# Performance work log

Measured on AMD Instinct MI355X. Metric: run time of the kernel, lower is better.

The kernel has to match this reference:

```python
import jax, jax.numpy as jnp
import numpy as np

D_MODEL = 128
D_STATE = 64
L = 1024
BATCH = 32
DT_MIN, DT_MAX = 1e-3, 1e-1

# poly6 Chebyshev coeffs for GELU on domain [-5, 15]
POLY6_GELU = [6.04831644882, 8.094460228971, 1.371512430522, -0.740775295685,
              0.134773988002, 0.126019270103, -0.239569101196]
GELU_LO, GELU_HI = -5.0, 15.0


def cheb_eval(x, coeffs, lo, hi):
    t = (2.0 * x - (hi + lo)) / (hi - lo)
    t0 = jnp.ones_like(t)
    res = coeffs[0] * t0
    t1 = t
    res = res + coeffs[1] * t1
    for i in range(2, len(coeffs)):
        ti = 2.0 * t * t1 - t0
        res = res + coeffs[i] * ti
        t0, t1 = t1, ti
    return res


def setup_inputs() -> dict:
    key = jax.random.key(0)
    ks = jax.random.split(key, 8)
    u = jax.random.normal(ks[0], (BATCH, D_MODEL, L), dtype=jnp.float32)
    # S4DKernel params
    log_dt = jax.random.uniform(ks[1], (D_MODEL,), dtype=jnp.float32) * (np.log(DT_MAX) - np.log(DT_MIN)) + np.log(DT_MIN)
    log_A_real = jnp.log(0.5 * jnp.ones((D_MODEL, D_STATE), dtype=jnp.float32))
    A_imag = jnp.pi * jnp.tile(jnp.arange(D_STATE, dtype=jnp.float32), (D_MODEL, 1))
    B_re = jnp.ones((D_MODEL, D_STATE), dtype=jnp.float32)
    B_im = jnp.zeros((D_MODEL, D_STATE), dtype=jnp.float32)
    C_re = jax.random.normal(ks[2], (D_MODEL, D_STATE), dtype=jnp.float32)
    C_im = jax.random.normal(ks[3], (D_MODEL, D_STATE), dtype=jnp.float32)
    # block params
    D = jax.random.normal(ks[4], (D_MODEL,), dtype=jnp.float32)
    W1 = jax.random.normal(ks[5], (2 * D_MODEL, D_MODEL), dtype=jnp.float32) * (1.0 / np.sqrt(D_MODEL))
    b1 = jnp.zeros((2 * D_MODEL,), dtype=jnp.float32)
    Wdec = jax.random.normal(ks[6], (1, D_MODEL), dtype=jnp.float32) * (1.0 / np.sqrt(D_MODEL))
    bdec = jnp.zeros((1,), dtype=jnp.float32)
    return {"u": u, "log_dt": log_dt, "log_A_real": log_A_real, "A_imag": A_imag,
            "B_re": B_re, "B_im": B_im, "C_re": C_re, "C_im": C_im,
            "D": D, "W1": W1, "b1": b1, "Wdec": Wdec, "bdec": bdec}


def s4d_kernel(log_dt, log_A_real, A_imag, B_re, B_im, C_re, C_im, length):
    dt = jnp.exp(log_dt)                                  # (d,)
    A = -jnp.exp(log_A_real) + 1j * A_imag                # (d, n) complex
    A_bar = jnp.exp(A * dt[:, None])                      # (d, n)
    Bc = B_re + 1j * B_im
    Cc = C_re + 1j * C_im
    B_bar = (A_bar - 1.0) / A * Bc                        # (d, n)
    t = jnp.arange(length, dtype=jnp.float32)
    # A_bar ** t for integer t == exp(A * dt * t)  (branch cut cancels at integers)
    A_bar_pow = jnp.exp((A * dt[:, None])[:, :, None] * t)  # (d, n, L)
    K = jnp.sum(Cc[:, :, None] * A_bar_pow * B_bar[:, :, None], axis=1)  # (d, L)
    return jnp.real(K).astype(jnp.float32)


def reference(u, log_dt, log_A_real, A_imag, B_re, B_im, C_re, C_im, D, W1, b1, Wdec, bdec):
    d_model = u.shape[1]
    length = u.shape[2]
    K = s4d_kernel(log_dt, log_A_real, A_imag, B_re, B_im, C_re, C_im, length)  # (d, L)
    # torch F.conv1d(padding=L-1, groups=d)[..., :L] == left-padded depthwise cross-correlation
    conv = jax.lax.conv_general_dilated(
        u, K[:, None, :], window_strides=(1,), padding=[(length - 1, 0)],
        dimension_numbers=("NCH", "OIH", "NCH"), feature_group_count=d_model)  # (B, d, L)
    skip = conv + u * D[:, None]
    post_gelu = cheb_eval(skip, POLY6_GELU, GELU_LO, GELU_HI)
    # 1x1 conv to 2*d channels
    pre_gate = jnp.einsum("od,bdl->bol", W1, post_gelu) + b1[None, :, None]  # (B, 2d, L)
    a, b = jnp.split(pre_gate, 2, axis=1)
    gate = jnp.clip(0.25 * b + 0.5, 0.0, 1.0)  # linear_gate GLU
    gated = a * gate                            # (B, d, L)
    pooled = gated.mean(axis=-1)                # (B, d)
    return pooled @ Wdec.T + bdec               # (B, 1)
```

## Files before the change

### kernel.cpp

```cpp
#include <hip/hip_runtime.h>
#include <hip/hip_bf16.h>
#include <math.h>

#define D_MODEL 128
#define D_STATE 64
#define LEN 1024
#define BATCH 32
#define KC_STRIDE 1056

typedef short short8 __attribute__((ext_vector_type(8)));
typedef short short4v __attribute__((ext_vector_type(4)));
typedef float f32x4 __attribute__((ext_vector_type(4)));

__device__ __forceinline__ float gelu_cheb(float x) {
    float t = (2.0f * x - 10.0f) * 0.05f;
    float r = 6.04831644882f + 8.094460228971f * t;
    float tm1 = 1.0f, tc = t;
    float t2 = 2.0f * t * tc - tm1; r += 1.371512430522f  * t2;
    float t3 = 2.0f * t * t2 - tc;  r += -0.740775295685f * t3;
    float t4 = 2.0f * t * t3 - t2;  r += 0.134773988002f  * t4;
    float t5 = 2.0f * t * t4 - t3;  r += 0.126019270103f  * t5;
    float t6 = 2.0f * t * t5 - t4;  r += -0.239569101196f * t6;
    return r;
}

__device__ __forceinline__ unsigned f2bf(float f) {
    unsigned u = __float_as_uint(f);
    return (u + 0x7FFFu + ((u >> 16) & 1u)) >> 16;
}

__device__ __forceinline__ float bf2f(short s) {
    return __uint_as_float(((unsigned)(unsigned short)s) << 16);
}

__global__ __launch_bounds__(256) void k_genK3(const float* __restrict__ log_dt,
                                               const float* __restrict__ log_A_real,
                                               const float* __restrict__ A_imag,
                                               const float* __restrict__ B_re,
                                               const float* __restrict__ B_im,
                                               const float* __restrict__ C_re,
                                               const float* __restrict__ C_im,
                                               const float* __restrict__ W1,
                                               const float* __restrict__ u,
                                               short* __restrict__ w1bf,
                                               short* __restrict__ u_bf,
                                               float* __restrict__ K) {
    __shared__ float Ls[128][68];
    int bid = blockIdx.x;
    int d = bid >> 3, oct = bid & 7;
    int t = threadIdx.x;

    if (t < 32) { int i = bid * 32 + t; w1bf[i] = (short)f2bf(W1[i]); }

    {
        size_t tid = (size_t)bid * 256 + t;
        const float4* src = (const float4*)(u + tid * 16);
        float4 a = src[0], b4 = src[1], c4 = src[2], d4 = src[3];
        uint4 o0, o1;
        o0.x = f2bf(a.x)  | (f2bf(a.y)  << 16);
        o0.y = f2bf(a.z)  | (f2bf(a.w)  << 16);
        o0.z = f2bf(b4.x) | (f2bf(b4.y) << 16);
        o0.w = f2bf(b4.z) | (f2bf(b4.w) << 16);
        o1.x = f2bf(c4.x) | (f2bf(c4.y) << 16);
        o1.y = f2bf(c4.z) | (f2bf(c4.w) << 16);
        o1.z = f2bf(d4.x) | (f2bf(d4.y) << 16);
        o1.w = f2bf(d4.z) | (f2bf(d4.w) << 16);
        uint4* dst = (uint4*)u_bf + tid * 2;
        dst[0] = o0; dst[1] = o1;
    }

    int w = t >> 6, lane = t & 63;
    int idx = d * D_STATE + lane;
    float dt  = expf(log_dt[d]);
    float Are = -expf(log_A_real[idx]);
    float Aim = A_imag[idx];
    float dre = Are * dt, dim = Aim * dt;
    float e = expf(dre);
    float sn, cs; sincosf(dim, &sn, &cs);
    float zre = e * cs, zim = e * sn;
    float numr = zre - 1.0f, numi = zim;
    float inv = 1.0f / (Are * Are + Aim * Aim);
    float qr = (numr * Are + numi * Aim) * inv;
    float qi = (numi * Are - numr * Aim) * inv;
    float Br = B_re[idx], Bi = B_im[idx];
    float Bbr = qr * Br - qi * Bi;
    float Bbi = qr * Bi + qi * Br;
    float Cr = C_re[idx], Ci = C_im[idx];
    float ar = Cr * Bbr - Ci * Bbi;
    float ai = Cr * Bbi + Ci * Bbr;

    int L0 = oct * 128 + w * 32;
    float fl0 = (float)L0;
    float pre = 0.f, pim = 0.f;
    if (dre * fl0 > -30.f) {
        float e0 = expf(dre * fl0);
        float s0, c0; sincosf(dim * fl0, &s0, &c0);
        pre = e0 * (ar * c0 - ai * s0);
        pim = e0 * (ar * s0 + ai * c0);
    }

    int row0 = w * 32;
#pragma unroll
    for (int r = 0; r < 32; ++r) {
        Ls[row0 + r][lane] = pre;
        float nre = pre * zre - pim * zim;
        pim = pre * zim + pim * zre;
        pre = nre;
    }
    __syncthreads();

    if (t < 128) {
        f32x4 s4 = (f32x4){0.f, 0.f, 0.f, 0.f};
#pragma unroll
        for (int c = 0; c < 16; ++c) s4 += *(const f32x4*)&Ls[t][4 * c];
        K[(size_t)d * LEN + oct * 128 + t] = s4.x + s4.y + s4.z + s4.w;
    }
}

__global__ __launch_bounds__(256) void k_conv3(const float* __restrict__ K,
                                               const short* __restrict__ u_bf,
                                               const float* __restrict__ Dp,
                                               short* __restrict__ pgT) {
    __shared__ __align__(16) short Kc[8 * KC_STRIDE];
    int bid = blockIdx.x;
    int d  = bid >> 3;
    int nh = (bid >> 2) & 1;
    int sq = bid & 3;
    int t = threadIdx.x;

    if (t < 160) {
        int c = t / 20, y = t - c * 20;
        ((unsigned*)&Kc[c * KC_STRIDE + 1016])[y] = 0u;
    }
    {
        const float* kp = K + (size_t)d * LEN;
        float4 kv = ((const float4*)kp)[t];
        float vals[4] = {kv.x, kv.y, kv.z, kv.w};
#pragma unroll
        for (int mm = 0; mm < 4; ++mm) {
            int ei = 4 * t + mm;
            short bv = (short)f2bf(vals[mm]);
#pragma unroll
            for (int c = 0; c < 8; ++c) {
                int x = ei - c;
                if (x >= 0) Kc[c * KC_STRIDE + x] = bv;
            }
        }
    }
    __syncthreads();

    int wvu = __builtin_amdgcn_readfirstlane(t >> 6);
    int lane = t & 63;
    int m16 = lane & 15, q = lane >> 4;
    int cc = (7 - m16) & 7;
    const short* Krow = Kc + cc * KC_STRIDE;
    const short* ub = u_bf + (((size_t)(nh * 16 + m16) * D_MODEL + d) << 10);

    int x0[4];
    f32x4 accv[4];
#pragma unroll
    for (int j = 0; j < 4; ++j) {
        int I = sq + 4 * (wvu + 4 * j);
        x0[j] = 1023 + 8 * q - 16 * I - m16 - cc;
        accv[j] = (f32x4){0.f, 0.f, 0.f, 0.f};
    }

    int ks_end = (sq + 4 * wvu + 48) / 2 + 1;
    if (ks_end > 32) ks_end = 32;
    for (int ks = 0; ks < ks_end; ++ks) {
        short8 bfrag = *(const short8*)&ub[32 * ks + 8 * q];
#pragma unroll
        for (int j = 0; j < 4; ++j) {
            int I = sq + 4 * (wvu + 4 * j);
            if (2 * ks <= I) {
                short8 afrag = *(const short8*)&Krow[x0[j] + 32 * ks];
                accv[j] = __builtin_amdgcn_mfma_f32_16x16x32_bf16(afrag, bfrag, accv[j], 0, 0, 0);
            }
        }
    }

    float Dd = Dp[d];
    int b = nh * 16 + m16;
#pragma unroll
    for (int j = 0; j < 4; ++j) {
        int I = sq + 4 * (wvu + 4 * j);
        int l0 = 16 * I + 4 * q;
        short4v us = *(const short4v*)&ub[l0];
        float v0 = gelu_cheb(accv[j][0] + bf2f(us[0]) * Dd);
        float v1 = gelu_cheb(accv[j][1] + bf2f(us[1]) * Dd);
        float v2 = gelu_cheb(accv[j][2] + bf2f(us[2]) * Dd);
        float v3 = gelu_cheb(accv[j][3] + bf2f(us[3]) * Dd);
        size_t basep = ((size_t)b * LEN + l0) * D_MODEL + d;
        pgT[basep + 0 * D_MODEL] = (short)f2bf(v0);
        pgT[basep + 1 * D_MODEL] = (short)f2bf(v1);
        pgT[basep + 2 * D_MODEL] = (short)f2bf(v2);
        pgT[basep + 3 * D_MODEL] = (short)f2bf(v3);
    }
}

__global__ __launch_bounds__(256) void k_glu_mfma(const short* __restrict__ pgT,
                                                  const short* __restrict__ w1bf,
                                                  const float* __restrict__ b1,
                                                  const float* __restrict__ Wdec,
                                                  float* __restrict__ acc2) {
    __shared__ float red[4];
    int b = blockIdx.y;
    int lc = blockIdx.x;
    int l0 = lc * 64;
    int t = threadIdx.x;
    int wv = t >> 6, lane = t & 63;
    int m = lane & 15, q = lane >> 4;

    const short* wA0 = w1bf + ((2 * wv + 0) * 16 + m) * D_MODEL;
    const short* wA1 = w1bf + ((2 * wv + 1) * 16 + m) * D_MODEL;

    short8 aA0[4], aA1[4], aB0[4], aB1[4];
#pragma unroll
    for (int kki = 0; kki < 4; ++kki) {
        int ko = kki * 32 + q * 8;
        aA0[kki] = *(const short8*)(wA0 + ko);
        aA1[kki] = *(const short8*)(wA1 + ko);
        aB0[kki] = *(const short8*)(wA0 + 128 * D_MODEL + ko);
        aB1[kki] = *(const short8*)(wA1 + 128 * D_MODEL + ko);
    }

    const short* pgb = pgT + ((size_t)b * LEN + l0) * D_MODEL;

    f32x4 accA[2][4], accB[2][4];
#pragma unroll
    for (int p = 0; p < 2; ++p)
#pragma unroll
        for (int nt = 0; nt < 4; ++nt) {
            accA[p][nt] = (f32x4){0.f, 0.f, 0.f, 0.f};
            accB[p][nt] = (f32x4){0.f, 0.f, 0.f, 0.f};
        }

#pragma unroll
    for (int kki = 0; kki < 4; ++kki) {
        int ko = kki * 32 + q * 8;
        short8 bfr[4];
#pragma unroll
        for (int nt = 0; nt < 4; ++nt)
            bfr[nt] = *(const short8*)&pgb[(size_t)(nt * 16 + m) * D_MODEL + ko];
#pragma unroll
        for (int nt = 0; nt < 4; ++nt) {
            accA[0][nt] = __builtin_amdgcn_mfma_f32_16x16x32_bf16(aA0[kki], bfr[nt], accA[0][nt], 0, 0, 0);
            accA[1][nt] = __builtin_amdgcn_mfma_f32_16x16x32_bf16(aA1[kki], bfr[nt], accA[1][nt], 0, 0, 0);
            accB[0][nt] = __builtin_amdgcn_mfma_f32_16x16x32_bf16(aB0[kki], bfr[nt], accB[0][nt], 0, 0, 0);
            accB[1][nt] = __builtin_amdgcn_mfma_f32_16x16x32_bf16(aB1[kki], bfr[nt], accB[1][nt], 0, 0, 0);
        }
    }

    float s = 0.f;
#pragma unroll
    for (int p = 0; p < 2; ++p) {
        int oA = (2 * wv + p) * 16 + q * 4;
#pragma unroll
        for (int r = 0; r < 4; ++r) {
            int o = oA + r;
            float wd  = Wdec[o];
            float ba  = b1[o];
            float bb1 = b1[o + 128];
#pragma unroll
            for (int nt = 0; nt < 4; ++nt) {
                float aa  = accA[p][nt][r] + ba;
                float bbv = accB[p][nt][r] + bb1;
                float g = fminf(fmaxf(0.25f * bbv + 0.5f, 0.f), 1.f);
                s += wd * aa * g;
            }
        }
    }
#pragma unroll
    for (int off = 32; off > 0; off >>= 1) s += __shfl_down(s, off, 64);
    if (lane == 0) red[wv] = s;
    __syncthreads();
    if (t == 0) acc2[b * 16 + lc] = red[0] + red[1] + red[2] + red[3];
}

__global__ void k_finish(const float* __restrict__ acc2, const float* __restrict__ bdec,
                         float* __restrict__ out) {
    int b = threadIdx.x;
    if (b < BATCH) {
        float s = 0.f;
#pragma unroll
        for (int c = 0; c < 16; ++c) s += acc2[b * 16 + c];
        out[b] = s * (1.0f / (float)LEN) + bdec[0];
    }
}

extern "C" void kernel_launch(void* const* d_in, const int* in_sizes, int n_in,
                              void* d_out, int out_size, void* d_ws, size_t ws_size,
                              hipStream_t stream) {
    const float* u          = (const float*)d_in[0];
    const float* log_dt     = (const float*)d_in[1];
    const float* log_A_real = (const float*)d_in[2];
    const float* A_imag     = (const float*)d_in[3];
    const float* B_re       = (const float*)d_in[4];
    const float* B_im       = (const float*)d_in[5];
    const float* C_re       = (const float*)d_in[6];
    const float* C_im       = (const float*)d_in[7];
    const float* Dp         = (const float*)d_in[8];
    const float* W1         = (const float*)d_in[9];
    const float* b1         = (const float*)d_in[10];
    const float* Wdec       = (const float*)d_in[11];
    const float* bdec       = (const float*)d_in[12];
    float* out = (float*)d_out;

    float* w = (float*)d_ws;
    float* K      = w;
    float* acc2   = K + (size_t)D_MODEL * LEN;
    short* u_bf   = (short*)(acc2 + 512);
    short* pgT    = u_bf + (size_t)BATCH * D_MODEL * LEN;
    short* w1bf   = pgT + (size_t)BATCH * LEN * D_MODEL;

    k_genK3<<<D_MODEL * 8, 256, 0, stream>>>(log_dt, log_A_real, A_imag, B_re, B_im,
                                             C_re, C_im, W1, u, w1bf, u_bf, K);
    k_conv3<<<D_MODEL * 8, 256, 0, stream>>>(K, u_bf, Dp, pgT);
    k_glu_mfma<<<dim3(16, BATCH), 256, 0, stream>>>(pgT, w1bf, b1, Wdec, acc2);
    k_finish<<<1, 64, 0, stream>>>(acc2, bdec, out);
}
```

Baseline: 136.0 us.

## Precompute shifted bf16 K copies globally and pair causal tiles in conv kernel

The shifted bf16 copies of the convolution kernel are now built once per channel by a separate expand kernel into global memory. Previously every conv block rebuilt them in shared memory. The conv kernel now handles 4 channels per block and pairs tile rows I and I+4 so the causal triangular work is balanced across waves. It also writes pgT as packed 4-channel vectors instead of scattered 2-byte stores. The trade-off is an extra launch, A-fragment reads from global/L2 instead of LDS, and higher register pressure from 8 accumulators.

```diff
diff --git a/kernel.cpp b/kernel.cpp
--- a/kernel.cpp
+++ b/kernel.cpp
@@ -6,11 +6,13 @@
 #define D_STATE 64
 #define LEN 1024
 #define BATCH 32
+#define KROW 1064
 #define KC_STRIDE 1056
 
 typedef short short8 __attribute__((ext_vector_type(8)));
 typedef short short4v __attribute__((ext_vector_type(4)));
 typedef float f32x4 __attribute__((ext_vector_type(4)));
+typedef float float4u __attribute__((ext_vector_type(4), aligned(4)));
 
 __device__ __forceinline__ float gelu_cheb(float x) {
     float t = (2.0f * x - 10.0f) * 0.05f;
@@ -113,88 +115,112 @@
         f32x4 s4 = (f32x4){0.f, 0.f, 0.f, 0.f};
 #pragma unroll
         for (int c = 0; c < 16; ++c) s4 += *(const f32x4*)&Ls[t][4 * c];
-        K[(size_t)d * LEN + oct * 128 + t] = s4.x + s4.y + s4.z + s4.w;
-    }
-}
-
-__global__ __launch_bounds__(256) void k_conv3(const float* __restrict__ K,
+        K[(size_t)d * KROW + oct * 128 + t] = s4.x + s4.y + s4.z + s4.w;
+    } else if (oct == 7 && t < 168) {
+        K[(size_t)d * KROW + 1024 + (t - 128)] = 0.f;
+    }
+}
+
+__global__ __launch_bounds__(256) void k_expand(const float* __restrict__ K,
+                                                short* __restrict__ Kc8) {
+    int d = blockIdx.x;
+    int t = threadIdx.x;
+    int c = t >> 5;
+    const float* kp = K + (size_t)d * KROW;
+    short* outp = Kc8 + ((size_t)d * 8 + c) * KC_STRIDE;
+    for (int i = (t & 31); i < 132; i += 32) {
+        float4u a = *(const float4u*)(kp + 8 * i + c);
+        float4u b = *(const float4u*)(kp + 8 * i + c + 4);
+        uint4 o;
+        o.x = f2bf(a.x) | (f2bf(a.y) << 16);
+        o.y = f2bf(a.z) | (f2bf(a.w) << 16);
+        o.z = f2bf(b.x) | (f2bf(b.y) << 16);
+        o.w = f2bf(b.z) | (f2bf(b.w) << 16);
+        *(uint4*)(outp + 8 * i) = o;
+    }
+}
+
+__global__ __launch_bounds__(256) void k_conv5(const short* __restrict__ Kc8,
                                                const short* __restrict__ u_bf,
                                                const float* __restrict__ Dp,
                                                short* __restrict__ pgT) {
-    __shared__ __align__(16) short Kc[8 * KC_STRIDE];
     int bid = blockIdx.x;
-    int d  = bid >> 3;
-    int nh = (bid >> 2) & 1;
-    int sq = bid & 3;
+    int dg = bid >> 4;
+    int nh = (bid >> 3) & 1;
+    int ls = bid & 7;
+    int d0 = dg * 4;
     int t = threadIdx.x;
-
-    if (t < 160) {
-        int c = t / 20, y = t - c * 20;
-        ((unsigned*)&Kc[c * KC_STRIDE + 1016])[y] = 0u;
-    }
-    {
-        const float* kp = K + (size_t)d * LEN;
-        float4 kv = ((const float4*)kp)[t];
-        float vals[4] = {kv.x, kv.y, kv.z, kv.w};
-#pragma unroll
-        for (int mm = 0; mm < 4; ++mm) {
-            int ei = 4 * t + mm;
-            short bv = (short)f2bf(vals[mm]);
-#pragma unroll
-            for (int c = 0; c < 8; ++c) {
-                int x = ei - c;
-                if (x >= 0) Kc[c * KC_STRIDE + x] = bv;
-            }
-        }
-    }
-    __syncthreads();
-
-    int wvu = __builtin_amdgcn_readfirstlane(t >> 6);
-    int lane = t & 63;
-    int m16 = lane & 15, q = lane >> 4;
+    int w = __builtin_amdgcn_readfirstlane(t >> 6);
+    int lane = t & 63, m16 = lane & 15, q = lane >> 4;
     int cc = (7 - m16) & 7;
-    const short* Krow = Kc + cc * KC_STRIDE;
-    const short* ub = u_bf + (((size_t)(nh * 16 + m16) * D_MODEL + d) << 10);
-
-    int x0[4];
-    f32x4 accv[4];
-#pragma unroll
-    for (int j = 0; j < 4; ++j) {
-        int I = sq + 4 * (wvu + 4 * j);
-        x0[j] = 1023 + 8 * q - 16 * I - m16 - cc;
-        accv[j] = (f32x4){0.f, 0.f, 0.f, 0.f};
-    }
-
-    int ks_end = (sq + 4 * wvu + 48) / 2 + 1;
-    if (ks_end > 32) ks_end = 32;
-    for (int ks = 0; ks < ks_end; ++ks) {
-        short8 bfrag = *(const short8*)&ub[32 * ks + 8 * q];
-#pragma unroll
-        for (int j = 0; j < 4; ++j) {
-            int I = sq + 4 * (wvu + 4 * j);
-            if (2 * ks <= I) {
-                short8 afrag = *(const short8*)&Krow[x0[j] + 32 * ks];
-                accv[j] = __builtin_amdgcn_mfma_f32_16x16x32_bf16(afrag, bfrag, accv[j], 0, 0, 0);
-            }
-        }
-    }
-
-    float Dd = Dp[d];
     int b = nh * 16 + m16;
-#pragma unroll
-    for (int j = 0; j < 4; ++j) {
-        int I = sq + 4 * (wvu + 4 * j);
+    int I1 = 8 * ls + w;
+    int x1 = 1023 + 8 * q - 16 * I1 - m16 - cc;
+
+    const short* A1p[4]; const short* A2p[4]; const short* Bp[4];
+    f32x4 acc1[4], acc2[4];
+#pragma unroll
+    for (int dd = 0; dd < 4; ++dd) {
+        const short* cb = Kc8 + ((size_t)(d0 + dd) * 8 + cc) * KC_STRIDE;
+        A1p[dd] = cb + x1;
+        A2p[dd] = cb + x1 - 64;
+        Bp[dd]  = u_bf + (((size_t)b * D_MODEL + d0 + dd) << 10) + 8 * q;
+        acc1[dd] = (f32x4){0.f, 0.f, 0.f, 0.f};
+        acc2[dd] = (f32x4){0.f, 0.f, 0.f, 0.f};
+    }
+
+    int ks1 = I1 / 2 + 1;
+    for (int ks = 0; ks < ks1; ++ks) {
+        int off = 32 * ks;
+        short8 bfr[4];
+#pragma unroll
+        for (int dd = 0; dd < 4; ++dd) bfr[dd] = *(const short8*)(Bp[dd] + off);
+#pragma unroll
+        for (int dd = 0; dd < 4; ++dd) {
+            short8 a1 = *(const short8*)(A1p[dd] + off);
+            acc1[dd] = __builtin_amdgcn_mfma_f32_16x16x32_bf16(a1, bfr[dd], acc1[dd], 0, 0, 0);
+        }
+#pragma unroll
+        for (int dd = 0; dd < 4; ++dd) {
+            short8 a2 = *(const short8*)(A2p[dd] + off);
+            acc2[dd] = __builtin_amdgcn_mfma_f32_16x16x32_bf16(a2, bfr[dd], acc2[dd], 0, 0, 0);
+        }
+    }
+#pragma unroll
+    for (int p2 = 0; p2 < 2; ++p2) {
+        int off = 32 * (ks1 + p2);
+#pragma unroll
+        for (int dd = 0; dd < 4; ++dd) {
+            short8 bfr = *(const short8*)(Bp[dd] + off);
+            short8 a2  = *(const short8*)(A2p[dd] + off);
+            acc2[dd] = __builtin_amdgcn_mfma_f32_16x16x32_bf16(a2, bfr, acc2[dd], 0, 0, 0);
+        }
+    }
+
+    float Dv[4];
+#pragma unroll
+    for (int dd = 0; dd < 4; ++dd) Dv[dd] = Dp[d0 + dd];
+
+#pragma unroll
+    for (int jj = 0; jj < 2; ++jj) {
+        int I = jj ? (I1 + 4) : I1;
         int l0 = 16 * I + 4 * q;
-        short4v us = *(const short4v*)&ub[l0];
-        float v0 = gelu_cheb(accv[j][0] + bf2f(us[0]) * Dd);
-        float v1 = gelu_cheb(accv[j][1] + bf2f(us[1]) * Dd);
-        float v2 = gelu_cheb(accv[j][2] + bf2f(us[2]) * Dd);
-        float v3 = gelu_cheb(accv[j][3] + bf2f(us[3]) * Dd);
-        size_t basep = ((size_t)b * LEN + l0) * D_MODEL + d;
-        pgT[basep + 0 * D_MODEL] = (short)f2bf(v0);
-        pgT[basep + 1 * D_MODEL] = (short)f2bf(v1);
-        pgT[basep + 2 * D_MODEL] = (short)f2bf(v2);
-        pgT[basep + 3 * D_MODEL] = (short)f2bf(v3);
+        const f32x4* accs = jj ? acc2 : acc1;
+        float v[4][4];
+#pragma unroll
+        for (int dd = 0; dd < 4; ++dd) {
+            short4v us = *(const short4v*)(Bp[dd] - 8 * q + l0);
+#pragma unroll
+            for (int r = 0; r < 4; ++r)
+                v[dd][r] = gelu_cheb(accs[dd][r] + bf2f(us[r]) * Dv[dd]);
+        }
+#pragma unroll
+        for (int r = 0; r < 4; ++r) {
+            short4v pk;
+            pk[0] = (short)f2bf(v[0][r]); pk[1] = (short)f2bf(v[1][r]);
+            pk[2] = (short)f2bf(v[2][r]); pk[3] = (short)f2bf(v[3][r]);
+            *(short4v*)(pgT + ((size_t)b * LEN + l0 + r) * D_MODEL + d0) = pk;
+        }
     }
 }
 
@@ -308,14 +334,16 @@
 
     float* w = (float*)d_ws;
     float* K      = w;
-    float* acc2   = K + (size_t)D_MODEL * LEN;
+    float* acc2   = K + (size_t)D_MODEL * KROW;
     short* u_bf   = (short*)(acc2 + 512);
     short* pgT    = u_bf + (size_t)BATCH * D_MODEL * LEN;
     short* w1bf   = pgT + (size_t)BATCH * LEN * D_MODEL;
+    short* Kc8    = w1bf + (size_t)2 * D_MODEL * D_MODEL;
 
     k_genK3<<<D_MODEL * 8, 256, 0, stream>>>(log_dt, log_A_real, A_imag, B_re, B_im,
                                              C_re, C_im, W1, u, w1bf, u_bf, K);
-    k_conv3<<<D_MODEL * 8, 256, 0, stream>>>(K, u_bf, Dp, pgT);
+    k_expand<<<D_MODEL, 256, 0, stream>>>(K, Kc8);
+    k_conv5<<<512, 256, 0, stream>>>(Kc8, u_bf, Dp, pgT);
     k_glu_mfma<<<dim3(16, BATCH), 256, 0, stream>>>(pgT, w1bf, b1, Wdec, acc2);
     k_finish<<<1, 64, 0, stream>>>(acc2, bdec, out);
 }
```

Measured after the change: 166.2 us. 22.2% more time.

## Rewrite causal conv with 32x32x16 MFMA tiles covering all batches per wave

Applied to the files above, without the earlier changes.

The depthwise causal convolution kernel now uses 32x32x16 bf16 MFMA, so one wave covers all 32 batch rows and a 32-sample output tile. The old version used 16x16x32 MFMA split across batch halves. K is stored with a zero-padded row stride, which lets the Toeplitz shared-memory staging use vectorized float4 loads and uint4 bf16 stores instead of scalar scatter writes. The aim is fewer MFMA instructions and B-fragment reloads, plus cheaper LDS setup. In exchange, work per wave is imbalanced: trip counts grow with the output tile index within each block.

```diff
diff --git a/kernel.cpp b/kernel.cpp
--- a/kernel.cpp
+++ b/kernel.cpp
@@ -6,11 +6,14 @@
 #define D_STATE 64
 #define LEN 1024
 #define BATCH 32
+#define KROW 1064
 #define KC_STRIDE 1056
 
 typedef short short8 __attribute__((ext_vector_type(8)));
 typedef short short4v __attribute__((ext_vector_type(4)));
 typedef float f32x4 __attribute__((ext_vector_type(4)));
+typedef float f32x16 __attribute__((ext_vector_type(16)));
+typedef float float4u __attribute__((ext_vector_type(4), aligned(4)));
 
 __device__ __forceinline__ float gelu_cheb(float x) {
     float t = (2.0f * x - 10.0f) * 0.05f;
@@ -113,88 +116,70 @@
         f32x4 s4 = (f32x4){0.f, 0.f, 0.f, 0.f};
 #pragma unroll
         for (int c = 0; c < 16; ++c) s4 += *(const f32x4*)&Ls[t][4 * c];
-        K[(size_t)d * LEN + oct * 128 + t] = s4.x + s4.y + s4.z + s4.w;
-    }
-}
-
-__global__ __launch_bounds__(256) void k_conv3(const float* __restrict__ K,
+        K[(size_t)d * KROW + oct * 128 + t] = s4.x + s4.y + s4.z + s4.w;
+    } else if (oct == 7 && t < 168) {
+        K[(size_t)d * KROW + 1024 + (t - 128)] = 0.f;
+    }
+}
+
+__global__ __launch_bounds__(256) void k_conv7(const float* __restrict__ K,
                                                const short* __restrict__ u_bf,
                                                const float* __restrict__ Dp,
                                                short* __restrict__ pgT) {
     __shared__ __align__(16) short Kc[8 * KC_STRIDE];
     int bid = blockIdx.x;
-    int d  = bid >> 3;
-    int nh = (bid >> 2) & 1;
-    int sq = bid & 3;
+    int d = bid >> 3, g = bid & 7;
     int t = threadIdx.x;
 
-    if (t < 160) {
-        int c = t / 20, y = t - c * 20;
-        ((unsigned*)&Kc[c * KC_STRIDE + 1016])[y] = 0u;
-    }
     {
-        const float* kp = K + (size_t)d * LEN;
-        float4 kv = ((const float4*)kp)[t];
-        float vals[4] = {kv.x, kv.y, kv.z, kv.w};
-#pragma unroll
-        for (int mm = 0; mm < 4; ++mm) {
-            int ei = 4 * t + mm;
-            short bv = (short)f2bf(vals[mm]);
-#pragma unroll
-            for (int c = 0; c < 8; ++c) {
-                int x = ei - c;
-                if (x >= 0) Kc[c * KC_STRIDE + x] = bv;
-            }
+        const float* kp = K + (size_t)d * KROW;
+        int c = t >> 5;
+        short* outp = Kc + c * KC_STRIDE;
+        for (int i = (t & 31); i < 132; i += 32) {
+            float4u a = *(const float4u*)(kp + 8 * i + c);
+            float4u b = *(const float4u*)(kp + 8 * i + c + 4);
+            uint4 o;
+            o.x = f2bf(a.x) | (f2bf(a.y) << 16);
+            o.y = f2bf(a.z) | (f2bf(a.w) << 16);
+            o.z = f2bf(b.x) | (f2bf(b.y) << 16);
+            o.w = f2bf(b.z) | (f2bf(b.w) << 16);
+            *(uint4*)(outp + 8 * i) = o;
         }
     }
     __syncthreads();
 
-    int wvu = __builtin_amdgcn_readfirstlane(t >> 6);
+    int w = __builtin_amdgcn_readfirstlane(t >> 6);
     int lane = t & 63;
-    int m16 = lane & 15, q = lane >> 4;
-    int cc = (7 - m16) & 7;
+    int mm = lane & 31, h = lane >> 5;
+    int I = g * 4 + w;
+    int cc = (7 - mm) & 7;
     const short* Krow = Kc + cc * KC_STRIDE;
-    const short* ub = u_bf + (((size_t)(nh * 16 + m16) * D_MODEL + d) << 10);
-
-    int x0[4];
-    f32x4 accv[4];
-#pragma unroll
-    for (int j = 0; j < 4; ++j) {
-        int I = sq + 4 * (wvu + 4 * j);
-        x0[j] = 1023 + 8 * q - 16 * I - m16 - cc;
-        accv[j] = (f32x4){0.f, 0.f, 0.f, 0.f};
-    }
-
-    int ks_end = (sq + 4 * wvu + 48) / 2 + 1;
-    if (ks_end > 32) ks_end = 32;
-    for (int ks = 0; ks < ks_end; ++ks) {
-        short8 bfrag = *(const short8*)&ub[32 * ks + 8 * q];
-#pragma unroll
-        for (int j = 0; j < 4; ++j) {
-            int I = sq + 4 * (wvu + 4 * j);
-            if (2 * ks <= I) {
-                short8 afrag = *(const short8*)&Krow[x0[j] + 32 * ks];
-                accv[j] = __builtin_amdgcn_mfma_f32_16x16x32_bf16(afrag, bfrag, accv[j], 0, 0, 0);
-            }
-        }
+    int x0 = 1023 + 8 * h - 32 * I - mm - cc;
+    const short* ubrow = u_bf + (((size_t)mm * D_MODEL + d) << 10);
+    const short* bp = ubrow + 8 * h;
+
+    f32x16 acc;
+#pragma unroll
+    for (int i = 0; i < 16; ++i) acc[i] = 0.f;
+
+    int trips = 2 * I + 2;
+    for (int ks = 0; ks < trips; ++ks) {
+        short8 afrag = *(const short8*)&Krow[x0 + 16 * ks];
+        short8 bfrag = *(const short8*)(bp + 16 * ks);
+        acc = __builtin_amdgcn_mfma_f32_32x32x16_bf16(afrag, bfrag, acc, 0, 0, 0);
     }
 
     float Dd = Dp[d];
-    int b = nh * 16 + m16;
-#pragma unroll
-    for (int j = 0; j < 4; ++j) {
-        int I = sq + 4 * (wvu + 4 * j);
-        int l0 = 16 * I + 4 * q;
-        short4v us = *(const short4v*)&ub[l0];
-        float v0 = gelu_cheb(accv[j][0] + bf2f(us[0]) * Dd);
-        float v1 = gelu_cheb(accv[j][1] + bf2f(us[1]) * Dd);
-        float v2 = gelu_cheb(accv[j][2] + bf2f(us[2]) * Dd);
-        float v3 = gelu_cheb(accv[j][3] + bf2f(us[3]) * Dd);
-        size_t basep = ((size_t)b * LEN + l0) * D_MODEL + d;
-        pgT[basep + 0 * D_MODEL] = (short)f2bf(v0);
-        pgT[basep + 1 * D_MODEL] = (short)f2bf(v1);
-        pgT[basep + 2 * D_MODEL] = (short)f2bf(v2);
-        pgT[basep + 3 * D_MODEL] = (short)f2bf(v3);
+    size_t pbase = ((size_t)mm * LEN + 32 * I) * D_MODEL + d;
+#pragma unroll
+    for (int rg = 0; rg < 4; ++rg) {
+        int lofs = 8 * rg + 4 * h;
+        short4v us = *(const short4v*)(ubrow + 32 * I + lofs);
+#pragma unroll
+        for (int rr = 0; rr < 4; ++rr) {
+            float v = gelu_cheb(acc[rg * 4 + rr] + bf2f(us[rr]) * Dd);
+            pgT[pbase + (size_t)(lofs + rr) * D_MODEL] = (short)f2bf(v);
+        }
     }
 }
 
@@ -308,14 +293,14 @@
 
     float* w = (float*)d_ws;
     float* K      = w;
-    float* acc2   = K + (size_t)D_MODEL * LEN;
+    float* acc2   = K + (size_t)D_MODEL * KROW;
     short* u_bf   = (short*)(acc2 + 512);
     short* pgT    = u_bf + (size_t)BATCH * D_MODEL * LEN;
     short* w1bf   = pgT + (size_t)BATCH * LEN * D_MODEL;
 
     k_genK3<<<D_MODEL * 8, 256, 0, stream>>>(log_dt, log_A_real, A_imag, B_re, B_im,
                                              C_re, C_im, W1, u, w1bf, u_bf, K);
-    k_conv3<<<D_MODEL * 8, 256, 0, stream>>>(K, u_bf, Dp, pgT);
+    k_conv7<<<D_MODEL * 8, 256, 0, stream>>>(K, u_bf, Dp, pgT);
     k_glu_mfma<<<dim3(16, BATCH), 256, 0, stream>>>(pgT, w1bf, b1, Wdec, acc2);
     k_finish<<<1, 64, 0, stream>>>(acc2, bdec, out);
 }
```

After: 150.7 us. +10.8%, slower.
